# Kernel optimization log

Measured on AMD Instinct MI355X. Metric: run time of the kernel, lower is better.

The kernel has to match this reference:

```python
import jax, jax.numpy as jnp
import numpy as np

B, T, D = 2, 1024, 1024
H = 16            # n_head
E = 8             # num_experts
TOPK = 2
F = 4 * D         # fc_rate * embed_dim
EPS = 1e-5


def _ln(x, g, b):
    mu = jnp.mean(x, axis=-1, keepdims=True)
    var = jnp.mean(jnp.square(x - mu), axis=-1, keepdims=True)
    return (x - mu) * jax.lax.rsqrt(var + EPS) * g + b


def setup_inputs() -> dict:
    key = jax.random.key(0)
    ks = jax.random.split(key, 24)
    s = 0.02
    return {
        "hidden_states": jax.random.normal(ks[0], (B, T, D), jnp.float32),
        "noise": jax.random.normal(ks[1], (B * T, E), jnp.float32),
        "ln1_g": jnp.ones((D,), jnp.float32), "ln1_b": jnp.zeros((D,), jnp.float32),
        "ln2_g": jnp.ones((D,), jnp.float32), "ln2_b": jnp.zeros((D,), jnp.float32),
        "wq": jax.random.normal(ks[2], (D, D), jnp.float32) * s, "bq": jnp.zeros((D,), jnp.float32),
        "wk": jax.random.normal(ks[3], (D, D), jnp.float32) * s, "bk": jnp.zeros((D,), jnp.float32),
        "wv": jax.random.normal(ks[4], (D, D), jnp.float32) * s, "bv": jnp.zeros((D,), jnp.float32),
        "wp": jax.random.normal(ks[5], (D, D), jnp.float32) * s, "bp": jnp.zeros((D,), jnp.float32),
        "wg": jax.random.normal(ks[6], (D, E), jnp.float32) * s, "bg": jnp.zeros((E,), jnp.float32),
        "wn": jax.random.normal(ks[7], (D, E), jnp.float32) * s, "bn": jnp.zeros((E,), jnp.float32),
        "w_in": jax.random.normal(ks[8], (E, D, F), jnp.float32) * s,
        "b_in": jnp.zeros((E, F), jnp.float32),
        "w_out": jax.random.normal(ks[9], (E, F, D), jnp.float32) * s,
        "b_out": jnp.zeros((E, D), jnp.float32),
    }


def reference(hidden_states, noise, ln1_g, ln1_b, ln2_g, ln2_b,
              wq, bq, wk, bk, wv, bv, wp, bp,
              wg, bg, wn, bn, w_in, b_in, w_out, b_out):
    x = hidden_states
    # ---- causal self-attention (dropout = eval / identity) ----
    h = _ln(x, ln1_g, ln1_b)
    dh = D // H
    q = (h @ wq + bq).reshape(B, T, H, dh)
    k = (h @ wk + bk).reshape(B, T, H, dh)
    v = (h @ wv + bv).reshape(B, T, H, dh)
    att = jnp.einsum('bthd,bshd->bhts', q, k) / jnp.sqrt(jnp.float32(dh))
    causal = jnp.tril(jnp.ones((T, T), bool))
    att = jnp.where(causal, att, -jnp.inf)
    att = jax.nn.softmax(att, axis=-1)
    y = jnp.einsum('bhts,bshd->bthd', att, v).reshape(B, T, D)
    x1 = x + (y @ wp + bp)
    # ---- noisy top-k MoE ----
    h2 = _ln(x1, ln2_g, ln2_b).reshape(B * T, D)
    gate_logits = h2 @ wg + bg                       # [N,E]
    noise_logits = h2 @ wn + bn
    noisy_logits = gate_logits + noise * jax.nn.softplus(noise_logits)
    rw = jax.nn.softmax(noisy_logits.astype(jnp.float32), axis=1)
    rw_top, sel = jax.lax.top_k(rw, TOPK)            # [N,k]
    rw_top = rw_top / jnp.sum(rw_top, axis=-1, keepdims=True)
    rw_top = rw_top.astype(h2.dtype)
    N = B * T
    # per-token combine weight for each expert (scatter of top-k weights)
    cw = jnp.zeros((N, E), h2.dtype).at[jnp.arange(N)[:, None], sel].add(rw_top)
    # dense grouped expert FFN: Linear -> exact GELU -> Linear (dropout=identity)
    mid = jax.nn.gelu(jnp.einsum('nd,edf->enf', h2, w_in) + b_in[:, None, :], approximate=False)
    exp_out = jnp.einsum('enf,efd->end', mid, w_out) + b_out[:, None, :]
    moe = jnp.einsum('ne,end->nd', cw, exp_out).reshape(B, T, D)
    # residual is the ORIGINAL layer input (as in the torch code)
    out = x + moe
    return (out, noisy_logits, gate_logits)
```

## Files before the change

kernel.cpp:

```cpp
#include <hip/hip_runtime.h>
#include <cmath>

typedef __attribute__((ext_vector_type(4))) float f4;
typedef __attribute__((ext_vector_type(8))) short s8;
typedef unsigned short u16;

#define N_TOK 2048
#define DIM   1024
#define NHEAD 16
#define DH    64
#define NE    8
#define FF    4096
#define SEQ   1024

__device__ __forceinline__ u16 f2bf(float f) {
    union { float fp; unsigned int u; } un; un.fp = f;
    unsigned int r = un.u + 0x7FFFu + ((un.u >> 16) & 1u);
    return (u16)(r >> 16);
}

__global__ __launch_bounds__(256) void transposeK(const float* __restrict__ in,
                                                  u16* __restrict__ outp,
                                                  int R, int C, long sInZ, long sOutZ) {
    in += (long)blockIdx.z * sInZ;
    outp += (long)blockIdx.z * sOutZ;
    __shared__ float tile[32][33];
    int c0 = blockIdx.x * 32, r0 = blockIdx.y * 32;
    int c = threadIdx.x & 31, rq = threadIdx.x >> 5;
#pragma unroll
    for (int p = 0; p < 4; p++)
        tile[rq + p * 8][c] = in[(long)(r0 + rq + p * 8) * C + c0 + c];
    __syncthreads();
#pragma unroll
    for (int p = 0; p < 4; p++) {
        int cc = rq + p * 8;
        outp[(long)(c0 + cc) * R + r0 + c] = f2bf(tile[c][cc]);
    }
}

__global__ void biaspack(const float* bq, const float* bk, const float* bv, float* dst) {
    int z = blockIdx.x;
    const float* s = (z == 0) ? bq : ((z == 1) ? bk : bv);
    for (int i = threadIdx.x; i < DIM; i += 256) dst[z * DIM + i] = s[i];
}

__global__ __launch_bounds__(256) void ln_kernel(const float* __restrict__ x,
                                                 const float* __restrict__ g,
                                                 const float* __restrict__ b,
                                                 u16* __restrict__ o) {
    int n = blockIdx.x, tid = threadIdx.x;
    f4 v = ((const f4*)(x + (long)n * DIM))[tid];
    float s = v.x + v.y + v.z + v.w;
    float ss = v.x * v.x + v.y * v.y + v.z * v.z + v.w * v.w;
    __shared__ float red[16];
#pragma unroll
    for (int off = 32; off; off >>= 1) { s += __shfl_down(s, off); ss += __shfl_down(ss, off); }
    int w = tid >> 6;
    if ((tid & 63) == 0) { red[w] = s; red[8 + w] = ss; }
    __syncthreads();
    s = red[0] + red[1] + red[2] + red[3];
    ss = red[8] + red[9] + red[10] + red[11];
    float mu = s * (1.0f / DIM);
    float var = ss * (1.0f / DIM) - mu * mu;
    float rstd = rsqrtf(var + 1e-5f);
    f4 gv = ((const f4*)g)[tid], bv = ((const f4*)b)[tid];
    ushort4 pk;
    pk.x = f2bf((v.x - mu) * rstd * gv.x + bv.x);
    pk.y = f2bf((v.y - mu) * rstd * gv.y + bv.y);
    pk.z = f2bf((v.z - mu) * rstd * gv.z + bv.z);
    pk.w = f2bf((v.w - mu) * rstd * gv.w + bv.w);
    ((ushort4*)(o + (long)n * DIM))[tid] = pk;
}

#define BM 128
#define BN 128
#define BK 32
#define LDK 40

template <int EPI, bool GATHER, bool USEOFF>
__global__ __launch_bounds__(256) void gemm_k(
    const u16* __restrict__ A, long strideAz,
    const u16* __restrict__ BT, long strideBz,
    const float* __restrict__ bias, long strideBiasz,
    float* __restrict__ Cf, u16* __restrict__ Cb, long strideCz,
    const float* __restrict__ res,
    const int* __restrict__ rowlist, int rlStride,
    const int* __restrict__ cnt_p, const int* __restrict__ off_p,
    int M, int N, int K) {
    int z = blockIdx.z;
    int Mv = cnt_p ? cnt_p[z] : M;
    int m0 = blockIdx.y * BM;
    if (m0 >= Mv) return;
    int n0 = blockIdx.x * BN;
    int off = (USEOFF && off_p) ? off_p[z] : 0;
    A += z * strideAz;
    BT += z * strideBz;
    bias += z * strideBiasz;

    __shared__ u16 As[BM * LDK];
    __shared__ u16 Bs[BN * LDK];

    int tid = threadIdx.x;
    int r0 = tid >> 2, seg = tid & 3;

    auto srcrow = [&](int r) -> long {
        int i = m0 + r;
        if (GATHER) {
            int ii = (i < Mv) ? rowlist[z * rlStride + i] : 0;
            return (long)ii;
        } else {
            int ii = (i < Mv) ? i : (Mv - 1);
            return (long)ii + (USEOFF ? (long)off : 0L);
        }
    };

    const u16* aSrc0 = A + srcrow(r0) * K + seg * 8;
    const u16* aSrc1 = A + srcrow(r0 + 64) * K + seg * 8;
    const u16* bSrc0 = BT + (long)(n0 + r0) * K + seg * 8;
    const u16* bSrc1 = BT + (long)(n0 + r0 + 64) * K + seg * 8;
    uint4* asD0 = (uint4*)(As + r0 * LDK + seg * 8);
    uint4* asD1 = (uint4*)(As + (r0 + 64) * LDK + seg * 8);
    uint4* bsD0 = (uint4*)(Bs + r0 * LDK + seg * 8);
    uint4* bsD1 = (uint4*)(Bs + (r0 + 64) * LDK + seg * 8);

    f4 acc[4][4] = {};
    int lane = tid & 63;
    int w = tid >> 6, wm = w & 1, wn = w >> 1;
    int fr = lane & 15, kq = (lane >> 4) * 8;

    for (int kb = 0; kb < K; kb += BK) {
        uint4 va0 = *(const uint4*)aSrc0; aSrc0 += BK;
        uint4 va1 = *(const uint4*)aSrc1; aSrc1 += BK;
        uint4 vb0 = *(const uint4*)bSrc0; bSrc0 += BK;
        uint4 vb1 = *(const uint4*)bSrc1; bSrc1 += BK;
        __syncthreads();
        *asD0 = va0; *asD1 = va1; *bsD0 = vb0; *bsD1 = vb1;
        __syncthreads();
        s8 af[4], bfv[4];
#pragma unroll
        for (int t = 0; t < 4; t++) {
            af[t]  = *(const s8*)(As + (wm * 64 + t * 16 + fr) * LDK + kq);
            bfv[t] = *(const s8*)(Bs + (wn * 64 + t * 16 + fr) * LDK + kq);
        }
#pragma unroll
        for (int mt = 0; mt < 4; mt++)
#pragma unroll
            for (int nt = 0; nt < 4; nt++)
                acc[mt][nt] = __builtin_amdgcn_mfma_f32_16x16x32_bf16(af[mt], bfv[nt], acc[mt][nt], 0, 0, 0);
    }

#pragma unroll
    for (int nt = 0; nt < 4; nt++) {
        int col = n0 + wn * 64 + nt * 16 + fr;
        float bv = bias[col];
#pragma unroll
        for (int mt = 0; mt < 4; mt++) {
            int rbase = m0 + wm * 64 + mt * 16 + (lane >> 4) * 4;
#pragma unroll
            for (int i = 0; i < 4; i++) {
                int rl = rbase + i;
                if (rl < Mv) {
                    float vvv = acc[mt][nt][i] + bv;
                    long crow = (long)rl + (USEOFF ? off : 0);
                    if (EPI == 0) {
                        Cf[z * strideCz + crow * N + col] = vvv;
                    } else if (EPI == 1) {
                        Cf[crow * (long)N + col] = vvv + res[crow * (long)N + col];
                    } else if (EPI == 2) {
                        float gl = 0.5f * vvv * (1.0f + erff(vvv * 0.70710678118654752f));
                        Cb[crow * (long)N + col] = f2bf(gl);
                    } else {
                        Cb[z * strideCz + crow * N + col] = f2bf(vvv);
                    }
                }
            }
        }
    }
}

#define ALDK 72

__global__ __launch_bounds__(256) void fattn_kernel(const u16* __restrict__ qkv,
                                                    u16* __restrict__ y) {
    __shared__ u16 Qs[128 * ALDK];
    __shared__ u16 Ks[64 * ALDK];
    __shared__ u16 Vs[64 * ALDK];
    __shared__ u16 Ps[4][32 * ALDK];
    int qt = blockIdx.x;
    int bh = blockIdx.y, b = bh >> 4, h = bh & 15;
    int tid = threadIdx.x, w = tid >> 6, lane = tid & 63;
    int fr = lane & 15, quad = lane >> 4;

    const u16* Qg = qkv + ((long)(b * SEQ + qt * 128) * DIM + h * DH);
    const u16* Kg = qkv + (long)N_TOK * DIM + ((long)b * SEQ * DIM + h * DH);
    const u16* Vg = Kg + (long)N_TOK * DIM;

#pragma unroll
    for (int p = 0; p < 4; p++) {
        int item = tid + p * 256;
        int r = item >> 3, seg = item & 7;
        *(uint4*)(Qs + r * ALDK + seg * 8) = *(const uint4*)(Qg + (long)r * DIM + seg * 8);
    }
    __syncthreads();

    s8 qf[2][2];
    int qrow = w * 32;
#pragma unroll
    for (int mt = 0; mt < 2; mt++)
#pragma unroll
        for (int kk = 0; kk < 2; kk++)
            qf[mt][kk] = *(const s8*)(Qs + (qrow + mt * 16 + fr) * ALDK + kk * 32 + quad * 8);

    f4 o_acc[2][4] = {};
    float m_run[2][4], l_run[2][4];
#pragma unroll
    for (int mt = 0; mt < 2; mt++)
#pragma unroll
        for (int i = 0; i < 4; i++) { m_run[mt][i] = -INFINITY; l_run[mt][i] = 0.f; }

    int qb_wave = qt * 128 + w * 32;
    int nkt = 2 * qt + 2;
    for (int kt = 0; kt < nkt; kt++) {
        __syncthreads();
#pragma unroll
        for (int p = 0; p < 2; p++) {
            int item = tid + p * 256;
            int r = item >> 3, seg = item & 7;
            *(uint4*)(Ks + r * ALDK + seg * 8) =
                *(const uint4*)(Kg + (long)(kt * 64 + r) * DIM + seg * 8);
            uint4 vv = *(const uint4*)(Vg + (long)(kt * 64 + r) * DIM + seg * 8);
            const u16* vp = (const u16*)&vv;
#pragma unroll
            for (int j = 0; j < 8; j++)
                Vs[(seg * 8 + j) * ALDK + r] = vp[j];
        }
        __syncthreads();

        bool act = (kt * 64 <= qb_wave + 31);
        if (act) {
            f4 s_acc[2][4] = {};
#pragma unroll
            for (int kk = 0; kk < 2; kk++) {
                s8 bf[4];
#pragma unroll
                for (int nt = 0; nt < 4; nt++)
                    bf[nt] = *(const s8*)(Ks + (nt * 16 + fr) * ALDK + kk * 32 + quad * 8);
#pragma unroll
                for (int mt = 0; mt < 2; mt++)
#pragma unroll
                    for (int nt = 0; nt < 4; nt++)
                        s_acc[mt][nt] = __builtin_amdgcn_mfma_f32_16x16x32_bf16(
                            qf[mt][kk], bf[nt], s_acc[mt][nt], 0, 0, 0);
            }
#pragma unroll
            for (int mt = 0; mt < 2; mt++)
#pragma unroll
                for (int i = 0; i < 4; i++) {
                    int t_ = qb_wave + mt * 16 + quad * 4 + i;
#pragma unroll
                    for (int nt = 0; nt < 4; nt++) {
                        int s_ = kt * 64 + nt * 16 + fr;
                        float sv = s_acc[mt][nt][i] * 0.125f;
                        s_acc[mt][nt][i] = (s_ <= t_) ? sv : -1e30f;
                    }
                }
#pragma unroll
            for (int mt = 0; mt < 2; mt++)
#pragma unroll
                for (int i = 0; i < 4; i++) {
                    float rm = s_acc[mt][0][i];
#pragma unroll
                    for (int nt = 1; nt < 4; nt++) rm = fmaxf(rm, s_acc[mt][nt][i]);
                    rm = fmaxf(rm, __shfl_xor(rm, 1));
                    rm = fmaxf(rm, __shfl_xor(rm, 2));
                    rm = fmaxf(rm, __shfl_xor(rm, 4));
                    rm = fmaxf(rm, __shfl_xor(rm, 8));
                    float mn = fmaxf(m_run[mt][i], rm);
                    float alpha = __expf(m_run[mt][i] - mn);
                    m_run[mt][i] = mn;
                    float rs = 0.f;
#pragma unroll
                    for (int nt = 0; nt < 4; nt++) {
                        float p = __expf(s_acc[mt][nt][i] - mn);
                        s_acc[mt][nt][i] = p;
                        rs += p;
                    }
                    rs += __shfl_xor(rs, 1);
                    rs += __shfl_xor(rs, 2);
                    rs += __shfl_xor(rs, 4);
                    rs += __shfl_xor(rs, 8);
                    l_run[mt][i] = alpha * l_run[mt][i] + rs;
#pragma unroll
                    for (int dt = 0; dt < 4; dt++) o_acc[mt][dt][i] *= alpha;
                }
            u16* Pw = Ps[w];
#pragma unroll
            for (int mt = 0; mt < 2; mt++)
#pragma unroll
                for (int nt = 0; nt < 4; nt++)
#pragma unroll
                    for (int i = 0; i < 4; i++)
                        Pw[(mt * 16 + quad * 4 + i) * ALDK + nt * 16 + fr] =
                            f2bf(s_acc[mt][nt][i]);
        }
        __syncthreads();
        if (act) {
            u16* Pw = Ps[w];
#pragma unroll
            for (int kk = 0; kk < 2; kk++) {
                s8 pf[2], vf[4];
#pragma unroll
                for (int mt = 0; mt < 2; mt++)
                    pf[mt] = *(const s8*)(Pw + (mt * 16 + fr) * ALDK + kk * 32 + quad * 8);
#pragma unroll
                for (int dt = 0; dt < 4; dt++)
                    vf[dt] = *(const s8*)(Vs + (dt * 16 + fr) * ALDK + kk * 32 + quad * 8);
#pragma unroll
                for (int mt = 0; mt < 2; mt++)
#pragma unroll
                    for (int dt = 0; dt < 4; dt++)
                        o_acc[mt][dt] = __builtin_amdgcn_mfma_f32_16x16x32_bf16(
                            pf[mt], vf[dt], o_acc[mt][dt], 0, 0, 0);
            }
        }
    }
#pragma unroll
    for (int mt = 0; mt < 2; mt++)
#pragma unroll
        for (int i = 0; i < 4; i++) {
            float linv = 1.0f / l_run[mt][i];
            int t_ = qt * 128 + w * 32 + mt * 16 + quad * 4 + i;
            u16* yrow = y + (long)(b * SEQ + t_) * DIM + h * DH;
#pragma unroll
            for (int dt = 0; dt < 4; dt++)
                yrow[dt * 16 + fr] = f2bf(o_acc[mt][dt][i] * linv);
        }
}

__global__ __launch_bounds__(256) void gate_kernel(
    const float* __restrict__ x1, const float* __restrict__ g, const float* __restrict__ b,
    const float* __restrict__ wg, const float* __restrict__ bg,
    const float* __restrict__ wn, const float* __restrict__ bn,
    const float* __restrict__ noise, u16* __restrict__ h2,
    float* __restrict__ out_noisy, float* __restrict__ out_gate,
    int* __restrict__ cnt, int* __restrict__ list,
    int* __restrict__ tokE, int* __restrict__ tokP, float* __restrict__ tokW) {
    __shared__ float hrow[DIM];
    __shared__ float red[256 * 16];
    __shared__ float red8[16];
    int n = blockIdx.x, tid = threadIdx.x;
    f4 v = ((const f4*)(x1 + (long)n * DIM))[tid];
    float s = v.x + v.y + v.z + v.w;
    float ss = v.x * v.x + v.y * v.y + v.z * v.z + v.w * v.w;
#pragma unroll
    for (int off = 32; off; off >>= 1) { s += __shfl_down(s, off); ss += __shfl_down(ss, off); }
    int wv_ = tid >> 6;
    if ((tid & 63) == 0) { red8[wv_] = s; red8[8 + wv_] = ss; }
    __syncthreads();
    s = red8[0] + red8[1] + red8[2] + red8[3];
    ss = red8[8] + red8[9] + red8[10] + red8[11];
    float mu = s * (1.0f / DIM);
    float var = ss * (1.0f / DIM) - mu * mu;
    float rstd = rsqrtf(var + 1e-5f);
    f4 gv = ((const f4*)g)[tid], bv = ((const f4*)b)[tid];
    float h0 = (v.x - mu) * rstd * gv.x + bv.x;
    float h1 = (v.y - mu) * rstd * gv.y + bv.y;
    float h2v = (v.z - mu) * rstd * gv.z + bv.z;
    float h3 = (v.w - mu) * rstd * gv.w + bv.w;
    hrow[tid * 4 + 0] = h0; hrow[tid * 4 + 1] = h1;
    hrow[tid * 4 + 2] = h2v; hrow[tid * 4 + 3] = h3;
    ushort4 pk;
    pk.x = f2bf(h0); pk.y = f2bf(h1); pk.z = f2bf(h2v); pk.w = f2bf(h3);
    ((ushort4*)(h2 + (long)n * DIM))[tid] = pk;
    __syncthreads();
    float ag[8] = {0, 0, 0, 0, 0, 0, 0, 0}, an[8] = {0, 0, 0, 0, 0, 0, 0, 0};
    for (int d = tid; d < DIM; d += 256) {
        float hv = hrow[d];
        const f4* wgp = (const f4*)(wg + (long)d * NE);
        f4 w0 = wgp[0], w1 = wgp[1];
        ag[0] += hv * w0.x; ag[1] += hv * w0.y; ag[2] += hv * w0.z; ag[3] += hv * w0.w;
        ag[4] += hv * w1.x; ag[5] += hv * w1.y; ag[6] += hv * w1.z; ag[7] += hv * w1.w;
        const f4* wnp = (const f4*)(wn + (long)d * NE);
        f4 n0v = wnp[0], n1v = wnp[1];
        an[0] += hv * n0v.x; an[1] += hv * n0v.y; an[2] += hv * n0v.z; an[3] += hv * n0v.w;
        an[4] += hv * n1v.x; an[5] += hv * n1v.y; an[6] += hv * n1v.z; an[7] += hv * n1v.w;
    }
#pragma unroll
    for (int j = 0; j < 8; j++) { red[tid * 16 + j] = ag[j]; red[tid * 16 + 8 + j] = an[j]; }
    __syncthreads();
    for (int st = 128; st > 0; st >>= 1) {
        if (tid < st) {
#pragma unroll
            for (int j = 0; j < 16; j++) red[tid * 16 + j] += red[(tid + st) * 16 + j];
        }
        __syncthreads();
    }
    if (tid == 0) {
        float gl[8], nl[8], ny[8];
#pragma unroll
        for (int e = 0; e < 8; e++) { gl[e] = red[e] + bg[e]; nl[e] = red[8 + e] + bn[e]; }
#pragma unroll
        for (int e = 0; e < 8; e++) {
            float xx = nl[e];
            float sp = (xx > 20.f) ? xx : log1pf(expf(xx));
            ny[e] = gl[e] + noise[(long)n * 8 + e] * sp;
        }
#pragma unroll
        for (int e = 0; e < 8; e++) {
            out_noisy[(long)n * 8 + e] = ny[e];
            out_gate[(long)n * 8 + e] = gl[e];
        }
        float mx = ny[0];
#pragma unroll
        for (int e = 1; e < 8; e++) mx = fmaxf(mx, ny[e]);
        float p[8], sum = 0.f;
#pragma unroll
        for (int e = 0; e < 8; e++) { p[e] = expf(ny[e] - mx); sum += p[e]; }
        int e1 = 0;
#pragma unroll
        for (int e = 1; e < 8; e++) if (p[e] > p[e1]) e1 = e;
        int e2 = (e1 == 0) ? 1 : 0;
#pragma unroll
        for (int e = 0; e < 8; e++) if (e != e1 && p[e] > p[e2]) e2 = e;
        float wsum = p[e1] + p[e2];
        float w1 = p[e1] / wsum, w2 = p[e2] / wsum;
        int q1 = atomicAdd(&cnt[e1], 1);
        list[e1 * N_TOK + q1] = n; tokE[2 * n] = e1; tokP[2 * n] = q1; tokW[2 * n] = w1;
        int q2 = atomicAdd(&cnt[e2], 1);
        list[e2 * N_TOK + q2] = n; tokE[2 * n + 1] = e2; tokP[2 * n + 1] = q2; tokW[2 * n + 1] = w2;
    }
}

__global__ void offs_kernel(const int* __restrict__ cnt, int* __restrict__ off) {
    if (threadIdx.x == 0) {
        int a = 0;
#pragma unroll
        for (int e = 0; e < NE; e++) { off[e] = a; a += cnt[e]; }
    }
}

__global__ __launch_bounds__(256) void combine_kernel(
    const float* __restrict__ x, const float* __restrict__ C2, const int* __restrict__ offp,
    const int* __restrict__ tokE, const int* __restrict__ tokP, const float* __restrict__ tokW,
    float* __restrict__ out) {
    int n = blockIdx.x, tid = threadIdx.x;
    int e0 = tokE[2 * n], e1 = tokE[2 * n + 1];
    long s0 = (long)offp[e0] + tokP[2 * n];
    long s1 = (long)offp[e1] + tokP[2 * n + 1];
    float w0 = tokW[2 * n], w1 = tokW[2 * n + 1];
    f4 xv = ((const f4*)(x + (long)n * DIM))[tid];
    f4 a = ((const f4*)(C2 + s0 * DIM))[tid];
    f4 b = ((const f4*)(C2 + s1 * DIM))[tid];
    f4 o = xv + w0 * a + w1 * b;
    ((f4*)(out + (long)n * DIM))[tid] = o;
}

extern "C" void kernel_launch(void* const* d_in, const int* in_sizes, int n_in,
                              void* d_out, int out_size, void* d_ws, size_t ws_size,
                              hipStream_t stream) {
    (void)in_sizes; (void)n_in; (void)out_size; (void)ws_size;
    const float* x     = (const float*)d_in[0];
    const float* noise = (const float*)d_in[1];
    const float* ln1g  = (const float*)d_in[2];
    const float* ln1b  = (const float*)d_in[3];
    const float* ln2g  = (const float*)d_in[4];
    const float* ln2b  = (const float*)d_in[5];
    const float* wq = (const float*)d_in[6];  const float* bq = (const float*)d_in[7];
    const float* wk = (const float*)d_in[8];  const float* bk = (const float*)d_in[9];
    const float* wv = (const float*)d_in[10]; const float* bv = (const float*)d_in[11];
    const float* wp = (const float*)d_in[12]; const float* bp = (const float*)d_in[13];
    const float* wg = (const float*)d_in[14]; const float* bg = (const float*)d_in[15];
    const float* wn = (const float*)d_in[16]; const float* bn = (const float*)d_in[17];
    const float* w_in  = (const float*)d_in[18]; const float* b_in  = (const float*)d_in[19];
    const float* w_out = (const float*)d_in[20]; const float* b_out = (const float*)d_in[21];
    float* out = (float*)d_out;

    char* ws = (char*)d_ws;
    size_t o = 0;
    auto alloc = [&](size_t sz) -> char* { char* p = ws + o; o += (sz + 255) & ~(size_t)255; return p; };
    u16*   hB    = (u16*)alloc((size_t)N_TOK * DIM * 2);
    u16*   wT    = (u16*)alloc(4ull * DIM * DIM * 2);
    u16*   qkvB  = (u16*)alloc(3ull * N_TOK * DIM * 2);
    u16*   yB    = (u16*)alloc((size_t)N_TOK * DIM * 2);
    float* x1    = (float*)alloc((size_t)N_TOK * DIM * 4);
    u16*   h2B   = (u16*)alloc((size_t)N_TOK * DIM * 2);
    u16*   winT  = (u16*)alloc((size_t)NE * DIM * FF * 2);
    u16*   woutT = (u16*)alloc((size_t)NE * DIM * FF * 2);
    u16*   mid   = (u16*)alloc((size_t)N_TOK * 2 * FF * 2);
    float* C2    = (float*)alloc((size_t)N_TOK * 2 * DIM * 4);
    float* qkvb  = (float*)alloc(3ull * DIM * 4);
    int*   cnt   = (int*)alloc(NE * 4);
    int*   offp  = (int*)alloc(NE * 4);
    int*   list  = (int*)alloc((size_t)NE * N_TOK * 4);
    int*   tokE  = (int*)alloc((size_t)N_TOK * 2 * 4);
    int*   tokP  = (int*)alloc((size_t)N_TOK * 2 * 4);
    float* tokW  = (float*)alloc((size_t)N_TOK * 2 * 4);

    transposeK<<<dim3(32, 32, 1), 256, 0, stream>>>(wq, wT + 0ull * DIM * DIM, DIM, DIM, 0, 0);
    transposeK<<<dim3(32, 32, 1), 256, 0, stream>>>(wk, wT + 1ull * DIM * DIM, DIM, DIM, 0, 0);
    transposeK<<<dim3(32, 32, 1), 256, 0, stream>>>(wv, wT + 2ull * DIM * DIM, DIM, DIM, 0, 0);
    transposeK<<<dim3(32, 32, 1), 256, 0, stream>>>(wp, wT + 3ull * DIM * DIM, DIM, DIM, 0, 0);
    transposeK<<<dim3(FF / 32, DIM / 32, NE), 256, 0, stream>>>(w_in, winT, DIM, FF, (long)DIM * FF, (long)DIM * FF);
    transposeK<<<dim3(DIM / 32, FF / 32, NE), 256, 0, stream>>>(w_out, woutT, FF, DIM, (long)DIM * FF, (long)DIM * FF);
    biaspack<<<dim3(3), 256, 0, stream>>>(bq, bk, bv, qkvb);

    ln_kernel<<<dim3(N_TOK), 256, 0, stream>>>(x, ln1g, ln1b, hB);
    gemm_k<3, false, false><<<dim3(DIM / BN, N_TOK / BM, 3), 256, 0, stream>>>(
        hB, 0, wT, (long)DIM * DIM, qkvb, DIM, nullptr, qkvB, (long)N_TOK * DIM,
        nullptr, nullptr, 0, nullptr, nullptr, N_TOK, DIM, DIM);
    fattn_kernel<<<dim3(SEQ / 128, 2 * NHEAD), 256, 0, stream>>>(qkvB, yB);
    gemm_k<1, false, false><<<dim3(DIM / BN, N_TOK / BM, 1), 256, 0, stream>>>(
        yB, 0, wT + 3ull * DIM * DIM, 0, bp, 0, x1, nullptr, 0,
        x, nullptr, 0, nullptr, nullptr, N_TOK, DIM, DIM);
    hipMemsetAsync(cnt, 0, NE * sizeof(int), stream);
    gate_kernel<<<dim3(N_TOK), 256, 0, stream>>>(
        x1, ln2g, ln2b, wg, bg, wn, bn, noise, h2B,
        out + 2097152, out + 2097152 + 16384,
        cnt, list, tokE, tokP, tokW);
    offs_kernel<<<dim3(1), 64, 0, stream>>>(cnt, offp);
    gemm_k<2, true, true><<<dim3(FF / BN, N_TOK / BM, NE), 256, 0, stream>>>(
        h2B, 0, winT, (long)DIM * FF, b_in, FF, nullptr, mid, 0,
        nullptr, list, N_TOK, cnt, offp, N_TOK, FF, DIM);
    gemm_k<0, false, true><<<dim3(DIM / BN, N_TOK / BM, NE), 256, 0, stream>>>(
        mid, 0, woutT, (long)DIM * FF, b_out, DIM, C2, nullptr, 0,
        nullptr, nullptr, 0, cnt, offp, N_TOK, DIM, FF);
    combine_kernel<<<dim3(N_TOK), 256, 0, stream>>>(x, C2, offp, tokE, tokP, tokW, out);
}
```

Baseline: 834.4 us.

## Double-buffer GEMM LDS, add narrow N tiles and split-K with reduction

The GEMM now keeps two LDS buffers and prefetches global tiles two iterations ahead, so there is one barrier per K step instead of two. The tile width is a template parameter: the QKV and output projections use 64-wide N tiles to launch more blocks. The attention-projection and expert down-projection GEMMs use split-K by 2, with a separate reduction kernel that adds the partial sums and the residual. This trades extra partial-sum memory traffic and kernel launches for better occupancy, and the second split buffer reuses the qkvB allocation as scratch.

```diff
diff --git a/kernel.cpp b/kernel.cpp
--- a/kernel.cpp
+++ b/kernel.cpp
@@ -73,32 +73,35 @@
 }
 
 #define BM 128
-#define BN 128
 #define BK 32
 #define LDK 40
 
-template <int EPI, bool GATHER, bool USEOFF>
+template <int EPI, bool GATHER, bool USEOFF, int BNT, int SPLITK>
 __global__ __launch_bounds__(256) void gemm_k(
     const u16* __restrict__ A, long strideAz,
     const u16* __restrict__ BT, long strideBz,
     const float* __restrict__ bias, long strideBiasz,
-    float* __restrict__ Cf, u16* __restrict__ Cb, long strideCz,
+    float* __restrict__ Cf, u16* __restrict__ Cb, long strideCz, long splitStride,
     const float* __restrict__ res,
     const int* __restrict__ rowlist, int rlStride,
     const int* __restrict__ cnt_p, const int* __restrict__ off_p,
     int M, int N, int K) {
+    constexpr int NTv = BNT / 32;
     int z = blockIdx.z;
-    int Mv = cnt_p ? cnt_p[z] : M;
+    int ze = z / SPLITK, zs = z % SPLITK;
+    int Mv = cnt_p ? cnt_p[ze] : M;
     int m0 = blockIdx.y * BM;
     if (m0 >= Mv) return;
-    int n0 = blockIdx.x * BN;
-    int off = (USEOFF && off_p) ? off_p[z] : 0;
-    A += z * strideAz;
-    BT += z * strideBz;
-    bias += z * strideBiasz;
-
-    __shared__ u16 As[BM * LDK];
-    __shared__ u16 Bs[BN * LDK];
+    int n0 = blockIdx.x * BNT;
+    int off = (USEOFF && off_p) ? off_p[ze] : 0;
+    A += ze * strideAz;
+    BT += ze * strideBz;
+    bias += ze * strideBiasz;
+    int Ksp = K / SPLITK;
+    int ks = zs * Ksp;
+
+    __shared__ u16 As[2][BM * LDK];
+    __shared__ u16 Bs[2][BNT * LDK];
 
     int tid = threadIdx.x;
     int r0 = tid >> 2, seg = tid & 3;
@@ -106,7 +109,7 @@
     auto srcrow = [&](int r) -> long {
         int i = m0 + r;
         if (GATHER) {
-            int ii = (i < Mv) ? rowlist[z * rlStride + i] : 0;
+            int ii = (i < Mv) ? rowlist[ze * rlStride + i] : 0;
             return (long)ii;
         } else {
             int ii = (i < Mv) ? i : (Mv - 1);
@@ -114,48 +117,62 @@
         }
     };
 
-    const u16* aSrc0 = A + srcrow(r0) * K + seg * 8;
-    const u16* aSrc1 = A + srcrow(r0 + 64) * K + seg * 8;
-    const u16* bSrc0 = BT + (long)(n0 + r0) * K + seg * 8;
-    const u16* bSrc1 = BT + (long)(n0 + r0 + 64) * K + seg * 8;
-    uint4* asD0 = (uint4*)(As + r0 * LDK + seg * 8);
-    uint4* asD1 = (uint4*)(As + (r0 + 64) * LDK + seg * 8);
-    uint4* bsD0 = (uint4*)(Bs + r0 * LDK + seg * 8);
-    uint4* bsD1 = (uint4*)(Bs + (r0 + 64) * LDK + seg * 8);
-
-    f4 acc[4][4] = {};
+    const u16* aBase0 = A + srcrow(r0) * K + ks + seg * 8;
+    const u16* aBase1 = A + srcrow(r0 + 64) * K + ks + seg * 8;
+    const u16* bBase0 = BT + (long)(n0 + r0) * K + ks + seg * 8;
+    const u16* bBase1 = (BNT == 128) ? (BT + (long)(n0 + r0 + 64) * K + ks + seg * 8) : nullptr;
+
+    uint4 va0, va1, vb0, vb1;
+    auto loadg = [&](int it) {
+        long d = (long)it * BK;
+        va0 = *(const uint4*)(aBase0 + d);
+        va1 = *(const uint4*)(aBase1 + d);
+        vb0 = *(const uint4*)(bBase0 + d);
+        if (BNT == 128) vb1 = *(const uint4*)(bBase1 + d);
+    };
+    auto storlds = [&](int buf) {
+        *(uint4*)(As[buf] + r0 * LDK + seg * 8) = va0;
+        *(uint4*)(As[buf] + (r0 + 64) * LDK + seg * 8) = va1;
+        *(uint4*)(Bs[buf] + r0 * LDK + seg * 8) = vb0;
+        if (BNT == 128) *(uint4*)(Bs[buf] + (r0 + 64) * LDK + seg * 8) = vb1;
+    };
+
+    int nIter = Ksp / BK;
+    loadg(0);
+    storlds(0);
+    if (nIter > 1) loadg(1);
+
+    f4 acc[4][NTv] = {};
     int lane = tid & 63;
     int w = tid >> 6, wm = w & 1, wn = w >> 1;
-    int fr = lane & 15, kq = (lane >> 4) * 8;
-
-    for (int kb = 0; kb < K; kb += BK) {
-        uint4 va0 = *(const uint4*)aSrc0; aSrc0 += BK;
-        uint4 va1 = *(const uint4*)aSrc1; aSrc1 += BK;
-        uint4 vb0 = *(const uint4*)bSrc0; bSrc0 += BK;
-        uint4 vb1 = *(const uint4*)bSrc1; bSrc1 += BK;
+    int fr = lane & 15, quad = lane >> 4, kq = quad * 8;
+
+    for (int i = 0; i < nIter; i++) {
         __syncthreads();
-        *asD0 = va0; *asD1 = va1; *bsD0 = vb0; *bsD1 = vb1;
-        __syncthreads();
-        s8 af[4], bfv[4];
-#pragma unroll
-        for (int t = 0; t < 4; t++) {
-            af[t]  = *(const s8*)(As + (wm * 64 + t * 16 + fr) * LDK + kq);
-            bfv[t] = *(const s8*)(Bs + (wn * 64 + t * 16 + fr) * LDK + kq);
-        }
+        int cur = i & 1;
+        s8 af[4], bfv[NTv];
+#pragma unroll
+        for (int t = 0; t < 4; t++)
+            af[t] = *(const s8*)(As[cur] + (wm * 64 + t * 16 + fr) * LDK + kq);
+#pragma unroll
+        for (int t = 0; t < NTv; t++)
+            bfv[t] = *(const s8*)(Bs[cur] + (wn * (BNT / 2) + t * 16 + fr) * LDK + kq);
+        if (i + 1 < nIter) storlds(1 - cur);
+        if (i + 2 < nIter) loadg(i + 2);
 #pragma unroll
         for (int mt = 0; mt < 4; mt++)
 #pragma unroll
-            for (int nt = 0; nt < 4; nt++)
+            for (int nt = 0; nt < NTv; nt++)
                 acc[mt][nt] = __builtin_amdgcn_mfma_f32_16x16x32_bf16(af[mt], bfv[nt], acc[mt][nt], 0, 0, 0);
     }
 
 #pragma unroll
-    for (int nt = 0; nt < 4; nt++) {
-        int col = n0 + wn * 64 + nt * 16 + fr;
-        float bv = bias[col];
+    for (int nt = 0; nt < NTv; nt++) {
+        int col = n0 + wn * (BNT / 2) + nt * 16 + fr;
+        float bv = (SPLITK == 1 || zs == 0) ? bias[col] : 0.0f;
 #pragma unroll
         for (int mt = 0; mt < 4; mt++) {
-            int rbase = m0 + wm * 64 + mt * 16 + (lane >> 4) * 4;
+            int rbase = m0 + wm * 64 + mt * 16 + quad * 4;
 #pragma unroll
             for (int i = 0; i < 4; i++) {
                 int rl = rbase + i;
@@ -163,19 +180,27 @@
                     float vvv = acc[mt][nt][i] + bv;
                     long crow = (long)rl + (USEOFF ? off : 0);
                     if (EPI == 0) {
-                        Cf[z * strideCz + crow * N + col] = vvv;
-                    } else if (EPI == 1) {
-                        Cf[crow * (long)N + col] = vvv + res[crow * (long)N + col];
+                        Cf[(long)zs * splitStride + ze * strideCz + crow * N + col] = vvv;
                     } else if (EPI == 2) {
                         float gl = 0.5f * vvv * (1.0f + erff(vvv * 0.70710678118654752f));
                         Cb[crow * (long)N + col] = f2bf(gl);
                     } else {
-                        Cb[z * strideCz + crow * N + col] = f2bf(vvv);
+                        Cb[ze * strideCz + crow * (long)N + col] = f2bf(vvv);
                     }
                 }
             }
         }
     }
+}
+
+__global__ __launch_bounds__(256) void reduceK(const float* __restrict__ P, long sp,
+                                               const float* __restrict__ res,
+                                               float* __restrict__ o, int total4) {
+    int i = blockIdx.x * 256 + threadIdx.x;
+    if (i >= total4) return;
+    f4 v = ((const f4*)P)[i] + ((const f4*)(P + sp))[i];
+    if (res) v += ((const f4*)res)[i];
+    ((f4*)o)[i] = v;
 }
 
 #define ALDK 72
@@ -505,24 +530,31 @@
     biaspack<<<dim3(3), 256, 0, stream>>>(bq, bk, bv, qkvb);
 
     ln_kernel<<<dim3(N_TOK), 256, 0, stream>>>(x, ln1g, ln1b, hB);
-    gemm_k<3, false, false><<<dim3(DIM / BN, N_TOK / BM, 3), 256, 0, stream>>>(
-        hB, 0, wT, (long)DIM * DIM, qkvb, DIM, nullptr, qkvB, (long)N_TOK * DIM,
+    gemm_k<3, false, false, 64, 1><<<dim3(DIM / 64, N_TOK / BM, 3), 256, 0, stream>>>(
+        hB, 0, wT, (long)DIM * DIM, qkvb, DIM, nullptr, qkvB, (long)N_TOK * DIM, 0,
         nullptr, nullptr, 0, nullptr, nullptr, N_TOK, DIM, DIM);
     fattn_kernel<<<dim3(SEQ / 128, 2 * NHEAD), 256, 0, stream>>>(qkvB, yB);
-    gemm_k<1, false, false><<<dim3(DIM / BN, N_TOK / BM, 1), 256, 0, stream>>>(
-        yB, 0, wT + 3ull * DIM * DIM, 0, bp, 0, x1, nullptr, 0,
-        x, nullptr, 0, nullptr, nullptr, N_TOK, DIM, DIM);
+    gemm_k<0, false, false, 64, 2><<<dim3(DIM / 64, N_TOK / BM, 2), 256, 0, stream>>>(
+        yB, 0, wT + 3ull * DIM * DIM, 0, bp, 0, C2, nullptr, 0, (long)N_TOK * DIM,
+        nullptr, nullptr, 0, nullptr, nullptr, N_TOK, DIM, DIM);
+    reduceK<<<dim3(N_TOK * DIM / 4 / 256), 256, 0, stream>>>(
+        C2, (long)N_TOK * DIM, x, x1, N_TOK * DIM / 4);
     hipMemsetAsync(cnt, 0, NE * sizeof(int), stream);
     gate_kernel<<<dim3(N_TOK), 256, 0, stream>>>(
         x1, ln2g, ln2b, wg, bg, wn, bn, noise, h2B,
         out + 2097152, out + 2097152 + 16384,
         cnt, list, tokE, tokP, tokW);
     offs_kernel<<<dim3(1), 64, 0, stream>>>(cnt, offp);
-    gemm_k<2, true, true><<<dim3(FF / BN, N_TOK / BM, NE), 256, 0, stream>>>(
-        h2B, 0, winT, (long)DIM * FF, b_in, FF, nullptr, mid, 0,
+    gemm_k<2, true, true, 128, 1><<<dim3(FF / 128, N_TOK / BM, NE), 256, 0, stream>>>(
+        h2B, 0, winT, (long)DIM * FF, b_in, FF, nullptr, mid, 0, 0,
         nullptr, list, N_TOK, cnt, offp, N_TOK, FF, DIM);
-    gemm_k<0, false, true><<<dim3(DIM / BN, N_TOK / BM, NE), 256, 0, stream>>>(
-        mid, 0, woutT, (long)DIM * FF, b_out, DIM, C2, nullptr, 0,
-        nullptr, nullptr, 0, cnt, offp, N_TOK, DIM, FF);
+    {
+        long s1off = (long)((float*)qkvB - C2);
+        gemm_k<0, false, true, 64, 2><<<dim3(DIM / 64, N_TOK / BM, NE * 2), 256, 0, stream>>>(
+            mid, 0, woutT, (long)DIM * FF, b_out, DIM, C2, nullptr, 0, s1off,
+            nullptr, nullptr, 0, cnt, offp, N_TOK, DIM, FF);
+        reduceK<<<dim3(2 * N_TOK * DIM / 4 / 256), 256, 0, stream>>>(
+            C2, s1off, nullptr, C2, 2 * N_TOK * DIM / 4);
+    }
     combine_kernel<<<dim3(N_TOK), 256, 0, stream>>>(x, C2, offp, tokE, tokP, tokW, out);
 }
```

Result: faster. 744.5 us (-10.8%).
